# Performance work log

Hardware: AMD Instinct MI355X
Metric: run time of the kernel (lower is better)

The kernel has to match this reference:

```python
import jax, jax.numpy as jnp
import numpy as np

MAX_DELTAS = 4  # number of concurrently loaded delta adapters


def _dequant(qw, qz, sc):
    """GPTQ-style 4-bit dequant with a single group (g_idx == 0).

    qw: [D, O, K//8] int32, 8 x 4-bit values packed along the input (K) dim.
    qz: [D, O//8, 1] int32, 8 x 4-bit zero points packed along the output dim.
    sc: [D, O, 1] float scales (one group).
    Returns dense delta weights [D, O, K].
    """
    shifts = jnp.arange(8, dtype=jnp.int32) * 4
    D, O, Kp = qw.shape
    w = ((qw[:, :, :, None] >> shifts) & 0xF).reshape(D, O, Kp * 8)   # [D,O,K]
    z = ((qz[:, :, 0][:, :, None] >> shifts) & 0xF).reshape(D, O)     # [D,O]
    return (w.astype(sc.dtype) - (z.astype(sc.dtype) + 1.0)[:, :, None]) * sc


def setup_inputs() -> dict:
    key = jax.random.key(0)
    ks = jax.random.split(key, 16)
    T, IN = 1024, 4096
    Q, KV = 4096, 1024  # 32 q-heads, 8 kv-heads, head_size 128
    OUT = Q + 2 * KV    # 6144
    D, PACK = MAX_DELTAS, 8
    IMAX = np.int32(2**31 - 1)
    return {
        "x": jax.random.normal(ks[0], (T, IN), dtype=jnp.float32),
        "w_base": jax.random.normal(ks[1], (OUT, IN), dtype=jnp.float32) * 0.02,
        "bias": jax.random.normal(ks[2], (OUT,), dtype=jnp.float32) * 0.02,
        "qweight_q": jax.random.randint(ks[3], (D, Q, IN // PACK), 0, IMAX, dtype=jnp.int32),
        "qweight_k": jax.random.randint(ks[4], (D, KV, IN // PACK), 0, IMAX, dtype=jnp.int32),
        "qweight_v": jax.random.randint(ks[5], (D, KV, IN // PACK), 0, IMAX, dtype=jnp.int32),
        "qzeros_q": jax.random.randint(ks[6], (D, Q // PACK, 1), 0, IMAX, dtype=jnp.int32),
        "qzeros_k": jax.random.randint(ks[7], (D, KV // PACK, 1), 0, IMAX, dtype=jnp.int32),
        "qzeros_v": jax.random.randint(ks[8], (D, KV // PACK, 1), 0, IMAX, dtype=jnp.int32),
        "scales_q": jax.random.uniform(ks[9], (D, Q, 1), dtype=jnp.float32) * 0.01,
        "scales_k": jax.random.uniform(ks[10], (D, KV, 1), dtype=jnp.float32) * 0.01,
        "scales_v": jax.random.uniform(ks[11], (D, KV, 1), dtype=jnp.float32) * 0.01,
        "indices": jax.random.randint(ks[12], (T,), 0, D, dtype=jnp.int32),
    }


def reference(x, w_base, bias, qweight_q, qweight_k, qweight_v,
              qzeros_q, qzeros_k, qzeros_v, scales_q, scales_k, scales_v,
              indices):
    # Base fused QKV projection.
    out = x @ w_base.T + bias  # [T, OUT]
    # Dequantize the three packed delta stacks and concatenate along out dim,
    # matching the (q, k, v) output_slices scatter of apply_delta.
    Wd = jnp.concatenate([
        _dequant(qweight_q, qzeros_q, scales_q),
        _dequant(qweight_k, qzeros_k, scales_k),
        _dequant(qweight_v, qzeros_v, scales_v),
    ], axis=1)  # [D, OUT, IN]
    # Per-token indexed delta matmul: token t uses adapter indices[t].
    for d in range(MAX_DELTAS):
        xm = jnp.where((indices == d)[:, None], x, 0.0)  # [T, IN]
        out = out + xm @ Wd[d].T
    return out
```

## Files before the change

kernel.cpp:

```cpp
#include <hip/hip_runtime.h>
#include <stdint.h>

#define T_TOK 1024
#define K_IN  4096
#define N_OUT 6144
#define N_Q   4096
#define N_KV  1024
#define N_D   4
#define KP    512

#define TM 64
#define TN 128
#define BK 64
#define NSTEPS (K_IN / BK)
#define PM_MAX 1280
#define MT (PM_MAX/TM)
#define NT (N_OUT/TN)
#define NBLK (NT * MT)

#define NB_WB ((N_OUT * K_IN / 8) / 256)
#define NB_RP (48 * 4 * 2 * 8)
#define NB_XP (PM_MAX * 2)

typedef __attribute__((ext_vector_type(8)))  short  short8;
typedef __attribute__((ext_vector_type(4)))  float  float4v;
typedef __attribute__((ext_vector_type(4)))  float  f32x4;
typedef __attribute__((ext_vector_type(4)))  uint   u32x4;

__device__ __forceinline__ ushort f2bf(float f) {
    uint32_t u = __float_as_uint(f);
    u = (u + 0x7FFFu + ((u >> 16) & 1u)) >> 16;
    return (ushort)u;
}
__device__ __forceinline__ uint pack2(ushort a, ushort b) {
    return (uint)a | ((uint)b << 16);
}

__device__ __forceinline__ short8 unpack_nib(uint q) {
    union { u32x4 u; short8 s; } r;
    uint t1 = q >> 8, t2 = q >> 16, t3 = q >> 24;
    r.u.x = ((q  & 0xFu) | ((q  & 0xF0u) << 12)) | 0x43004300u;
    r.u.y = ((t1 & 0xFu) | ((t1 & 0xF0u) << 12)) | 0x43004300u;
    r.u.z = ((t2 & 0xFu) | ((t2 & 0xF0u) << 12)) | 0x43004300u;
    r.u.w = ((t3 & 0xFu) | ((t3 & 0xF0u) << 12)) | 0x43004300u;
    return r.s;
}

__global__ void build_perm_kernel(const int* __restrict__ indices,
                                  int* __restrict__ perm,
                                  int* __restrict__ pofs) {
    __shared__ int cw[16][4];
    __shared__ int pw[16][4];
    __shared__ int ps[N_D + 1];
    int tid = threadIdx.x;
    for (int p = tid; p < PM_MAX; p += 1024) perm[p] = -1;

    int d = indices[tid];
    unsigned long long m[4];
    m[0] = __ballot(d == 0); m[1] = __ballot(d == 1);
    m[2] = __ballot(d == 2); m[3] = __ballot(d == 3);
    int lane = tid & 63, wv = tid >> 6;
    if (lane < 4) cw[wv][lane] = (int)__popcll(m[lane]);
    __syncthreads();
    if (tid == 0) {
        int tot[4] = {0, 0, 0, 0};
        for (int w = 0; w < 16; w++)
            for (int dd = 0; dd < 4; dd++) { pw[w][dd] = tot[dd]; tot[dd] += cw[w][dd]; }
        int run = 0;
        for (int dd = 0; dd < N_D; dd++) { ps[dd] = run; run += ((tot[dd] + TM - 1) / TM) * TM; }
        ps[N_D] = run;
        for (int dd = 0; dd <= N_D; dd++) pofs[dd] = ps[dd];
    }
    __syncthreads();
    unsigned long long lt = (1ull << lane) - 1ull;
    int rank = pw[wv][d] + (int)__popcll(m[d] & lt);
    perm[ps[d] + rank] = tid;
}

__global__ void prep_kernel(const float* __restrict__ w_base, ushort* __restrict__ wb16,
                            const int* __restrict__ qw_q, const int* __restrict__ qw_k,
                            const int* __restrict__ qw_v, uint* __restrict__ qp,
                            const float* __restrict__ x, const int* __restrict__ perm,
                            ushort* __restrict__ xp, float* __restrict__ rs) {
    __shared__ int slds[64 * 64];
    int tid = threadIdx.x;
    int b = blockIdx.x;

    if (b < NB_WB) {
        int id = b * 256 + tid;
        const f32x4* src = (const f32x4*)(w_base + (size_t)id * 8);
        f32x4 a = __builtin_nontemporal_load(src);
        f32x4 c = __builtin_nontemporal_load(src + 1);
        u32x4 packv;
        packv.x = pack2(f2bf(a.x), f2bf(a.y));
        packv.y = pack2(f2bf(a.z), f2bf(a.w));
        packv.z = pack2(f2bf(c.x), f2bf(c.y));
        packv.w = pack2(f2bf(c.z), f2bf(c.w));
        *(u32x4*)(wb16 + (size_t)id * 8) = packv;
        return;
    }
    b -= NB_WB;
    if (b < NB_RP) {
        int s8 = b & 7;
        int r  = b >> 3;
        int w2 = r & 1; r >>= 1;
        int d  = r & 3;
        int bn = r >> 2;
        const int* qw; int r0, Osec;
        if (bn < 32)      { qw = qw_q; r0 = bn * 128;        Osec = N_Q;  }
        else if (bn < 40) { qw = qw_k; r0 = (bn - 32) * 128; Osec = N_KV; }
        else              { qw = qw_v; r0 = (bn - 40) * 128; Osec = N_KV; }
#pragma unroll
        for (int k = 0; k < 4; k++) {
            int p   = k * 256 + tid;
            int row = p >> 4, c4 = p & 15;
            const int* src = qw + ((size_t)d * Osec + r0 + w2 * 64 + row) * KP + s8 * 64 + c4 * 4;
            *(u32x4*)&slds[row * 64 + c4 * 4] = *(const u32x4*)src;
        }
        __syncthreads();
        size_t obase = (size_t)b * 4096;
#pragma unroll
        for (int k = 0; k < 2; k++) {
            int p    = k * 256 + tid;
            int sl   = p >> 6, lane = p & 63;
            int quad = lane >> 4, l16 = lane & 15;
            uint pk[8];
#pragma unroll
            for (int e = 0; e < 8; e++) {
                int jj = e >> 1, h = e & 1;
                pk[e] = (uint)slds[(jj * 16 + l16) * 64 + sl * 8 + h * 4 + quad];
            }
            *(u32x4*)(qp + obase + (size_t)p * 8)     = *(u32x4*)&pk[0];
            *(u32x4*)(qp + obase + (size_t)p * 8 + 4) = *(u32x4*)&pk[4];
        }
        return;
    }
    b -= NB_RP;
    {
        int pm = b >> 1;
        int half = b & 1;
        int c0 = half * (K_IN / 2) + tid * 8;
        int tok = perm[pm];
        ushort res[8];
        if (tok < 0) {
#pragma unroll
            for (int j = 0; j < 8; j++) res[j] = 0;
        } else {
            const f32x4* src = (const f32x4*)(x + (size_t)tok * K_IN + c0);
            f32x4 a = __builtin_nontemporal_load(src);
            f32x4 c = __builtin_nontemporal_load(src + 1);
            float v[8] = {a.x, a.y, a.z, a.w, c.x, c.y, c.z, c.w};
#pragma unroll
            for (int j = 0; j < 8; j++) res[j] = f2bf(v[j]);
        }
        u32x4 packv;
        packv.x = pack2(res[0], res[1]); packv.y = pack2(res[2], res[3]);
        packv.z = pack2(res[4], res[5]); packv.w = pack2(res[6], res[7]);
        *(u32x4*)(xp + (size_t)pm * K_IN + c0) = packv;

        float ssum = 0.f;
#pragma unroll
        for (int j = 0; j < 8; j++) ssum += __uint_as_float((uint)res[j] << 16);
#pragma unroll
        for (int off = 32; off > 0; off >>= 1) ssum += __shfl_xor(ssum, off);
        float* wsum = (float*)slds;
        if ((tid & 63) == 0) wsum[tid >> 6] = ssum;
        __syncthreads();
        if (tid == 0) rs[pm * 2 + half] = wsum[0] + wsum[1] + wsum[2] + wsum[3];
    }
}

__global__ __launch_bounds__(256, 3) void gemm_kernel(
    const ushort* __restrict__ xp, const ushort* __restrict__ wb16,
    const uint* __restrict__ qp,
    const int* __restrict__ qz_q, const int* __restrict__ qz_k, const int* __restrict__ qz_v,
    const float* __restrict__ sc_q, const float* __restrict__ sc_k, const float* __restrict__ sc_v,
    const float* __restrict__ bias,
    const int* __restrict__ perm, const int* __restrict__ pofs,
    const float* __restrict__ rs,
    float* __restrict__ out) {

    __shared__ ushort As[2][TM * BK];
    __shared__ ushort Bs[2][TN * BK];

    int lin  = blockIdx.x;
    int low3 = lin & 7, rest = lin >> 3;
    int bm   = rest % MT, bq = rest / MT;
    int bn   = bq * 8 + low3;

    int m0 = bm * TM, n0 = bn * TN;
    int ptot = pofs[N_D];
    if (m0 >= ptot) return;
    int d = 0;
    while (d < N_D - 1 && m0 >= pofs[d + 1]) d++;

    int tid  = threadIdx.x;
    int lane = tid & 63;
    int wv   = tid >> 6;
    int wm   = (wv & 1) * 32;
    int wn   = (wv >> 1) * 64;
    int quad = lane >> 4;
    int l16  = lane & 15;
    int xa   = l16 & 7;

    const uint* qpw = qp + (((size_t)(bn * 4 + d) * 2 + (wv >> 1)) * 64 * 64 * 8)
                         + (size_t)lane * 8;

    const float4v zero4 = {0.f, 0.f, 0.f, 0.f};
    float4v acc_b[2][4], acc_d[2][4];
#pragma unroll
    for (int i = 0; i < 2; i++)
#pragma unroll
        for (int jj = 0; jj < 4; jj++) { acc_b[i][jj] = zero4; acc_d[i][jj] = zero4; }

    auto stage = [&](ushort* dstA, ushort* dstB, int k0) {
#pragma unroll
        for (int w = 0; w < 2; w++) {
            int p   = w * 256 + tid;
            int row = p >> 3;
            int ckl = (p & 7) ^ (row & 7);
            const ushort* ga = xp + (size_t)(m0 + row) * K_IN + k0 + ckl * 8;
            int base = (w * 256 + (tid & ~63)) * 8;
            __builtin_amdgcn_global_load_lds((const __attribute__((address_space(1))) void*)ga,
                                             (__attribute__((address_space(3))) void*)(dstA + base), 16, 0, 0);
        }
#pragma unroll
        for (int w = 0; w < 4; w++) {
            int p   = w * 256 + tid;
            int row = p >> 3;
            int ckl = (p & 7) ^ (row & 7);
            const ushort* gb = wb16 + (size_t)(n0 + row) * K_IN + k0 + ckl * 8;
            int base = (w * 256 + (tid & ~63)) * 8;
            __builtin_amdgcn_global_load_lds((const __attribute__((address_space(1))) void*)gb,
                                             (__attribute__((address_space(3))) void*)(dstB + base), 16, 0, 0);
        }
    };

    int buf = 0;
    stage(As[0], Bs[0], 0);
    uint q_cur[8];
    *(u32x4*)&q_cur[0] = *(const u32x4*)(qpw);
    *(u32x4*)&q_cur[4] = *(const u32x4*)(qpw + 4);
    __syncthreads();

    for (int s = 0; s < NSTEPS; s++) {
        uint q_nxt[8];
        if (s + 1 < NSTEPS) {
            stage(As[1 - buf], Bs[1 - buf], (s + 1) * BK);
            const uint* qn = qpw + (size_t)(s + 1) * 512;
            *(u32x4*)&q_nxt[0] = *(const u32x4*)(qn);
            *(u32x4*)&q_nxt[4] = *(const u32x4*)(qn + 4);
        }

        const ushort* Ab = As[buf];
        const ushort* Bb = Bs[buf];
#pragma unroll
        for (int kk = 0; kk < BK; kk += 32) {
            int h   = kk >> 5;
            int ckb = (kk >> 3) + quad;
            short8 a[2], b[4], bd[4];
#pragma unroll
            for (int i = 0; i < 2; i++)
                a[i] = *(const short8*)(Ab + (wm + i * 16 + l16) * BK + (ckb ^ xa) * 8);
#pragma unroll
            for (int jj = 0; jj < 4; jj++)
                b[jj] = *(const short8*)(Bb + (wn + jj * 16 + l16) * BK + (ckb ^ xa) * 8);
#pragma unroll
            for (int jj = 0; jj < 4; jj++)
                bd[jj] = unpack_nib(q_cur[jj * 2 + h]);
#pragma unroll
            for (int i = 0; i < 2; i++)
#pragma unroll
                for (int jj = 0; jj < 4; jj++) {
                    acc_b[i][jj] = __builtin_amdgcn_mfma_f32_16x16x32_bf16(a[i], b[jj],  acc_b[i][jj], 0, 0, 0);
                    acc_d[i][jj] = __builtin_amdgcn_mfma_f32_16x16x32_bf16(a[i], bd[jj], acc_d[i][jj], 0, 0, 0);
                }
        }
        __syncthreads();
#pragma unroll
        for (int e = 0; e < 8; e++) q_cur[e] = q_nxt[e];
        buf ^= 1;
    }

    const int* qz; const float* sc; int r0, Osec;
    if (n0 < N_Q)            { qz = qz_q; sc = sc_q; r0 = n0;                Osec = N_Q;  }
    else if (n0 < N_Q + N_KV){ qz = qz_k; sc = sc_k; r0 = n0 - N_Q;          Osec = N_KV; }
    else                     { qz = qz_v; sc = sc_v; r0 = n0 - (N_Q + N_KV); Osec = N_KV; }

    float s4[4], cc4[4], bv4[4];
#pragma unroll
    for (int jj = 0; jj < 4; jj++) {
        int rsec = r0 + wn + jj * 16 + l16;
        float sv = sc[(size_t)d * Osec + rsec];
        int   zq = qz[(size_t)d * (Osec >> 3) + (rsec >> 3)];
        int   z  = (zq >> ((rsec & 7) * 4)) & 0xF;
        s4[jj]  = sv;
        cc4[jj] = sv * (float)(129 + z);
        bv4[jj] = bias[n0 + wn + jj * 16 + l16];
    }
#pragma unroll
    for (int i = 0; i < 2; i++) {
        int toks[4]; float rsv[4];
#pragma unroll
        for (int r = 0; r < 4; r++) {
            int row = m0 + wm + i * 16 + quad * 4 + r;
            toks[r] = perm[row];
            rsv[r]  = rs[row * 2] + rs[row * 2 + 1];
        }
#pragma unroll
        for (int jj = 0; jj < 4; jj++) {
            int col = n0 + wn + jj * 16 + l16;
#pragma unroll
            for (int r = 0; r < 4; r++) {
                int tok = toks[r];
                if (tok >= 0) {
                    float v = bv4[jj] + acc_b[i][jj][r] + s4[jj] * acc_d[i][jj][r] - cc4[jj] * rsv[r];
                    out[(size_t)tok * N_OUT + col] = v;
                }
            }
        }
    }
}

extern "C" void kernel_launch(void* const* d_in, const int* in_sizes, int n_in,
                              void* d_out, int out_size, void* d_ws, size_t ws_size,
                              hipStream_t stream) {
    const float* x      = (const float*)d_in[0];
    const float* w_base = (const float*)d_in[1];
    const float* bias   = (const float*)d_in[2];
    const int*   qw_q   = (const int*)d_in[3];
    const int*   qw_k   = (const int*)d_in[4];
    const int*   qw_v   = (const int*)d_in[5];
    const int*   qz_q   = (const int*)d_in[6];
    const int*   qz_k   = (const int*)d_in[7];
    const int*   qz_v   = (const int*)d_in[8];
    const float* sc_q   = (const float*)d_in[9];
    const float* sc_k   = (const float*)d_in[10];
    const float* sc_v   = (const float*)d_in[11];
    const int*   indices= (const int*)d_in[12];
    float* out = (float*)d_out;

    char* ws = (char*)d_ws;
    ushort* wb16 = (ushort*)ws;
    size_t wb_bytes = (size_t)N_OUT * K_IN * 2;
    ushort* xp = (ushort*)(ws + wb_bytes);
    size_t xp_bytes = (size_t)PM_MAX * K_IN * 2;
    float* rsum = (float*)(ws + wb_bytes + xp_bytes);
    size_t rs_bytes = (size_t)PM_MAX * 2 * sizeof(float);
    int* perm = (int*)(ws + wb_bytes + xp_bytes + rs_bytes);
    int* pofs = perm + PM_MAX;
    uint* qp  = (uint*)(ws + wb_bytes + xp_bytes + rs_bytes + PM_MAX * 4 + 64);

    build_perm_kernel<<<1, 1024, 0, stream>>>(indices, perm, pofs);
    prep_kernel<<<NB_WB + NB_RP + NB_XP, 256, 0, stream>>>(
        w_base, wb16, qw_q, qw_k, qw_v, qp, x, perm, xp, rsum);
    gemm_kernel<<<NBLK, 256, 0, stream>>>(xp, wb16, qp,
        qz_q, qz_k, qz_v, sc_q, sc_k, sc_v, bias,
        perm, pofs, rsum, out);
}
```

Baseline: 413.4 us.

## Fuse base-weight bf16 conversion into GEMM by staging fp32 w_base directly

Removes the separate prep pass that converted w_base to bf16 in workspace; the GEMM now streams fp32 w_base tiles into LDS and converts to bf16 per fragment at read time. This saves a full write and reread of the bf16 weight copy, but doubles LDS footprint and global traffic for B per tile across all M-tiles, and occupancy hint drops from 3 to 2 blocks. Also rewrites nibble unpacking with byte-permute instructions to cut ALU work.

```diff
diff --git a/kernel.cpp b/kernel.cpp
--- a/kernel.cpp
+++ b/kernel.cpp
@@ -1,4 +1,5 @@
 #include <hip/hip_runtime.h>
+#include <hip/hip_bf16.h>
 #include <stdint.h>
 
 #define T_TOK 1024
@@ -18,7 +19,6 @@
 #define NT (N_OUT/TN)
 #define NBLK (NT * MT)
 
-#define NB_WB ((N_OUT * K_IN / 8) / 256)
 #define NB_RP (48 * 4 * 2 * 8)
 #define NB_XP (PM_MAX * 2)
 
@@ -35,14 +35,20 @@
 __device__ __forceinline__ uint pack2(ushort a, ushort b) {
     return (uint)a | ((uint)b << 16);
 }
+__device__ __forceinline__ uint cvt2(float lo, float hi) {
+    union { __hip_bfloat162 h2; uint u; } c;
+    c.h2 = __float22bfloat162_rn(make_float2(lo, hi));
+    return c.u;
+}
 
 __device__ __forceinline__ short8 unpack_nib(uint q) {
     union { u32x4 u; short8 s; } r;
-    uint t1 = q >> 8, t2 = q >> 16, t3 = q >> 24;
-    r.u.x = ((q  & 0xFu) | ((q  & 0xF0u) << 12)) | 0x43004300u;
-    r.u.y = ((t1 & 0xFu) | ((t1 & 0xF0u) << 12)) | 0x43004300u;
-    r.u.z = ((t2 & 0xFu) | ((t2 & 0xF0u) << 12)) | 0x43004300u;
-    r.u.w = ((t3 & 0xFu) | ((t3 & 0xF0u) << 12)) | 0x43004300u;
+    uint e = q & 0x0F0F0F0Fu;
+    uint o = (q >> 4) & 0x0F0F0F0Fu;
+    r.u.x = __builtin_amdgcn_perm(o, e, 0x0C040C00u) | 0x43004300u;
+    r.u.y = __builtin_amdgcn_perm(o, e, 0x0C050C01u) | 0x43004300u;
+    r.u.z = __builtin_amdgcn_perm(o, e, 0x0C060C02u) | 0x43004300u;
+    r.u.w = __builtin_amdgcn_perm(o, e, 0x0C070C03u) | 0x43004300u;
     return r.s;
 }
 
@@ -77,8 +83,7 @@
     perm[ps[d] + rank] = tid;
 }
 
-__global__ void prep_kernel(const float* __restrict__ w_base, ushort* __restrict__ wb16,
-                            const int* __restrict__ qw_q, const int* __restrict__ qw_k,
+__global__ void prep_kernel(const int* __restrict__ qw_q, const int* __restrict__ qw_k,
                             const int* __restrict__ qw_v, uint* __restrict__ qp,
                             const float* __restrict__ x, const int* __restrict__ perm,
                             ushort* __restrict__ xp, float* __restrict__ rs) {
@@ -86,20 +91,6 @@
     int tid = threadIdx.x;
     int b = blockIdx.x;
 
-    if (b < NB_WB) {
-        int id = b * 256 + tid;
-        const f32x4* src = (const f32x4*)(w_base + (size_t)id * 8);
-        f32x4 a = __builtin_nontemporal_load(src);
-        f32x4 c = __builtin_nontemporal_load(src + 1);
-        u32x4 packv;
-        packv.x = pack2(f2bf(a.x), f2bf(a.y));
-        packv.y = pack2(f2bf(a.z), f2bf(a.w));
-        packv.z = pack2(f2bf(c.x), f2bf(c.y));
-        packv.w = pack2(f2bf(c.z), f2bf(c.w));
-        *(u32x4*)(wb16 + (size_t)id * 8) = packv;
-        return;
-    }
-    b -= NB_WB;
     if (b < NB_RP) {
         int s8 = b & 7;
         int r  = b >> 3;
@@ -170,8 +161,8 @@
     }
 }
 
-__global__ __launch_bounds__(256, 3) void gemm_kernel(
-    const ushort* __restrict__ xp, const ushort* __restrict__ wb16,
+__global__ __launch_bounds__(256, 2) void gemm_kernel(
+    const ushort* __restrict__ xp, const float* __restrict__ w_base,
     const uint* __restrict__ qp,
     const int* __restrict__ qz_q, const int* __restrict__ qz_k, const int* __restrict__ qz_v,
     const float* __restrict__ sc_q, const float* __restrict__ sc_k, const float* __restrict__ sc_v,
@@ -181,7 +172,7 @@
     float* __restrict__ out) {
 
     __shared__ ushort As[2][TM * BK];
-    __shared__ ushort Bs[2][TN * BK];
+    __shared__ float  Bs[2][TN * BK];
 
     int lin  = blockIdx.x;
     int low3 = lin & 7, rest = lin >> 3;
@@ -202,6 +193,7 @@
     int quad = lane >> 4;
     int l16  = lane & 15;
     int xa   = l16 & 7;
+    int xb   = (l16 & 7) << 1;
 
     const uint* qpw = qp + (((size_t)(bn * 4 + d) * 2 + (wv >> 1)) * 64 * 64 * 8)
                          + (size_t)lane * 8;
@@ -213,7 +205,7 @@
 #pragma unroll
         for (int jj = 0; jj < 4; jj++) { acc_b[i][jj] = zero4; acc_d[i][jj] = zero4; }
 
-    auto stage = [&](ushort* dstA, ushort* dstB, int k0) {
+    auto stage = [&](ushort* dstA, float* dstB, int k0) {
 #pragma unroll
         for (int w = 0; w < 2; w++) {
             int p   = w * 256 + tid;
@@ -225,12 +217,12 @@
                                              (__attribute__((address_space(3))) void*)(dstA + base), 16, 0, 0);
         }
 #pragma unroll
-        for (int w = 0; w < 4; w++) {
+        for (int w = 0; w < 8; w++) {
             int p   = w * 256 + tid;
-            int row = p >> 3;
-            int ckl = (p & 7) ^ (row & 7);
-            const ushort* gb = wb16 + (size_t)(n0 + row) * K_IN + k0 + ckl * 8;
-            int base = (w * 256 + (tid & ~63)) * 8;
+            int row = p >> 4;
+            int ckl = (p & 15) ^ ((row & 7) << 1);
+            const float* gb = w_base + (size_t)(n0 + row) * K_IN + k0 + ckl * 4;
+            int base = (w * 256 + (tid & ~63)) * 4;
             __builtin_amdgcn_global_load_lds((const __attribute__((address_space(1))) void*)gb,
                                              (__attribute__((address_space(3))) void*)(dstB + base), 16, 0, 0);
         }
@@ -253,7 +245,7 @@
         }
 
         const ushort* Ab = As[buf];
-        const ushort* Bb = Bs[buf];
+        const float*  Bb = Bs[buf];
 #pragma unroll
         for (int kk = 0; kk < BK; kk += 32) {
             int h   = kk >> 5;
@@ -263,8 +255,16 @@
             for (int i = 0; i < 2; i++)
                 a[i] = *(const short8*)(Ab + (wm + i * 16 + l16) * BK + (ckb ^ xa) * 8);
 #pragma unroll
-            for (int jj = 0; jj < 4; jj++)
-                b[jj] = *(const short8*)(Bb + (wn + jj * 16 + l16) * BK + (ckb ^ xa) * 8);
+            for (int jj = 0; jj < 4; jj++) {
+                int pos = ((h << 3) + (quad << 1)) ^ xb;
+                const float* pB = Bb + (wn + jj * 16 + l16) * BK + pos * 4;
+                f32x4 f0 = *(const f32x4*)pB;
+                f32x4 f1 = *(const f32x4*)(pB + 4);
+                union { u32x4 u; short8 s8v; } bc;
+                bc.u.x = cvt2(f0.x, f0.y); bc.u.y = cvt2(f0.z, f0.w);
+                bc.u.z = cvt2(f1.x, f1.y); bc.u.w = cvt2(f1.z, f1.w);
+                b[jj] = bc.s8v;
+            }
 #pragma unroll
             for (int jj = 0; jj < 4; jj++)
                 bd[jj] = unpack_nib(q_cur[jj * 2 + h]);
@@ -341,20 +341,18 @@
     float* out = (float*)d_out;
 
     char* ws = (char*)d_ws;
-    ushort* wb16 = (ushort*)ws;
-    size_t wb_bytes = (size_t)N_OUT * K_IN * 2;
-    ushort* xp = (ushort*)(ws + wb_bytes);
+    ushort* xp = (ushort*)ws;
     size_t xp_bytes = (size_t)PM_MAX * K_IN * 2;
-    float* rsum = (float*)(ws + wb_bytes + xp_bytes);
+    float* rsum = (float*)(ws + xp_bytes);
     size_t rs_bytes = (size_t)PM_MAX * 2 * sizeof(float);
-    int* perm = (int*)(ws + wb_bytes + xp_bytes + rs_bytes);
+    int* perm = (int*)(ws + xp_bytes + rs_bytes);
     int* pofs = perm + PM_MAX;
-    uint* qp  = (uint*)(ws + wb_bytes + xp_bytes + rs_bytes + PM_MAX * 4 + 64);
+    uint* qp  = (uint*)(ws + xp_bytes + rs_bytes + PM_MAX * 4 + 64);
 
     build_perm_kernel<<<1, 1024, 0, stream>>>(indices, perm, pofs);
-    prep_kernel<<<NB_WB + NB_RP + NB_XP, 256, 0, stream>>>(
-        w_base, wb16, qw_q, qw_k, qw_v, qp, x, perm, xp, rsum);
-    gemm_kernel<<<NBLK, 256, 0, stream>>>(xp, wb16, qp,
+    prep_kernel<<<NB_RP + NB_XP, 256, 0, stream>>>(
+        qw_q, qw_k, qw_v, qp, x, perm, xp, rsum);
+    gemm_kernel<<<NBLK, 256, 0, stream>>>(xp, w_base, qp,
         qz_q, qz_k, qz_v, sc_q, sc_k, sc_v, bias,
         perm, pofs, rsum, out);
 }
```

Measured after the change: 465.8 us. +12.7%, slower.

## Triple-buffer LDS staging with explicit vmcnt waits and perm-based nibble unpack

Applied to the files above, without the earlier changes.

Replaces the double-buffered K loop with a three-stage LDS ring that keeps two tile loads in flight, unrolled by two with manual s_waitcnt vmcnt and raw s_barrier instead of __syncthreads. The packed delta weights are ping-ponged between two register sets. The 4-bit unpack now uses v_perm byte shuffles to cut ALU instructions. The third buffer adds LDS use, so launch bounds drop occupancy from 3 to 2 blocks per CU. The hand-counted vmcnt values risk race conditions if the count of outstanding loads is wrong.

```diff
diff --git a/kernel.cpp b/kernel.cpp
--- a/kernel.cpp
+++ b/kernel.cpp
@@ -38,11 +38,12 @@
 
 __device__ __forceinline__ short8 unpack_nib(uint q) {
     union { u32x4 u; short8 s; } r;
-    uint t1 = q >> 8, t2 = q >> 16, t3 = q >> 24;
-    r.u.x = ((q  & 0xFu) | ((q  & 0xF0u) << 12)) | 0x43004300u;
-    r.u.y = ((t1 & 0xFu) | ((t1 & 0xF0u) << 12)) | 0x43004300u;
-    r.u.z = ((t2 & 0xFu) | ((t2 & 0xF0u) << 12)) | 0x43004300u;
-    r.u.w = ((t3 & 0xFu) | ((t3 & 0xF0u) << 12)) | 0x43004300u;
+    uint e = q & 0x0F0F0F0Fu;
+    uint o = (q >> 4) & 0x0F0F0F0Fu;
+    r.u.x = __builtin_amdgcn_perm(o, e, 0x0C040C00u) | 0x43004300u;
+    r.u.y = __builtin_amdgcn_perm(o, e, 0x0C050C01u) | 0x43004300u;
+    r.u.z = __builtin_amdgcn_perm(o, e, 0x0C060C02u) | 0x43004300u;
+    r.u.w = __builtin_amdgcn_perm(o, e, 0x0C070C03u) | 0x43004300u;
     return r.s;
 }
 
@@ -170,7 +171,7 @@
     }
 }
 
-__global__ __launch_bounds__(256, 3) void gemm_kernel(
+__global__ __launch_bounds__(256, 2) void gemm_kernel(
     const ushort* __restrict__ xp, const ushort* __restrict__ wb16,
     const uint* __restrict__ qp,
     const int* __restrict__ qz_q, const int* __restrict__ qz_k, const int* __restrict__ qz_v,
@@ -180,8 +181,8 @@
     const float* __restrict__ rs,
     float* __restrict__ out) {
 
-    __shared__ ushort As[2][TM * BK];
-    __shared__ ushort Bs[2][TN * BK];
+    __shared__ ushort As[3][TM * BK];
+    __shared__ ushort Bs[3][TN * BK];
 
     int lin  = blockIdx.x;
     int low3 = lin & 7, rest = lin >> 3;
@@ -236,24 +237,13 @@
         }
     };
 
-    int buf = 0;
-    stage(As[0], Bs[0], 0);
-    uint q_cur[8];
-    *(u32x4*)&q_cur[0] = *(const u32x4*)(qpw);
-    *(u32x4*)&q_cur[4] = *(const u32x4*)(qpw + 4);
-    __syncthreads();
-
-    for (int s = 0; s < NSTEPS; s++) {
-        uint q_nxt[8];
-        if (s + 1 < NSTEPS) {
-            stage(As[1 - buf], Bs[1 - buf], (s + 1) * BK);
-            const uint* qn = qpw + (size_t)(s + 1) * 512;
-            *(u32x4*)&q_nxt[0] = *(const u32x4*)(qn);
-            *(u32x4*)&q_nxt[4] = *(const u32x4*)(qn + 4);
-        }
-
-        const ushort* Ab = As[buf];
-        const ushort* Bb = Bs[buf];
+    auto qload = [&](uint* qdst, int step) {
+        const uint* qn = qpw + (size_t)step * 512;
+        *(u32x4*)&qdst[0] = *(const u32x4*)(qn);
+        *(u32x4*)&qdst[4] = *(const u32x4*)(qn + 4);
+    };
+
+    auto compute = [&](const ushort* Ab, const ushort* Bb, const uint* qc) {
 #pragma unroll
         for (int kk = 0; kk < BK; kk += 32) {
             int h   = kk >> 5;
@@ -261,13 +251,13 @@
             short8 a[2], b[4], bd[4];
 #pragma unroll
             for (int i = 0; i < 2; i++)
-                a[i] = *(const short8*)(Ab + (wm + i * 16 + l16) * BK + (ckb ^ xa) * 8);
+                a[i] = *(const short8*)(Ab + (wm + i * 16 + l16) * BK + ((ckb ^ xa) * 8));
 #pragma unroll
             for (int jj = 0; jj < 4; jj++)
-                b[jj] = *(const short8*)(Bb + (wn + jj * 16 + l16) * BK + (ckb ^ xa) * 8);
+                b[jj] = *(const short8*)(Bb + (wn + jj * 16 + l16) * BK + ((ckb ^ xa) * 8));
 #pragma unroll
             for (int jj = 0; jj < 4; jj++)
-                bd[jj] = unpack_nib(q_cur[jj * 2 + h]);
+                bd[jj] = unpack_nib(qc[jj * 2 + h]);
 #pragma unroll
             for (int i = 0; i < 2; i++)
 #pragma unroll
@@ -276,10 +266,38 @@
                     acc_d[i][jj] = __builtin_amdgcn_mfma_f32_16x16x32_bf16(a[i], bd[jj], acc_d[i][jj], 0, 0, 0);
                 }
         }
-        __syncthreads();
-#pragma unroll
-        for (int e = 0; e < 8; e++) q_cur[e] = q_nxt[e];
-        buf ^= 1;
+    };
+
+    uint qA[8], qB[8];
+
+    qload(qA, 0);
+    stage(As[0], Bs[0], 0);
+    stage(As[1], Bs[1], BK);
+    asm volatile("s_waitcnt vmcnt(6)" ::: "memory");
+    __builtin_amdgcn_s_barrier();
+
+    int b0 = 0, b1 = 1, b2 = 2;
+#pragma unroll 1
+    for (int s = 0; s < NSTEPS; s += 2) {
+        qload(qB, s + 1);
+        __builtin_amdgcn_sched_barrier(0);
+        if (s + 2 < NSTEPS) stage(As[b2], Bs[b2], (s + 2) * BK);
+        compute(As[b0], Bs[b0], qA);
+        if (s < NSTEPS - 2)       asm volatile("s_waitcnt vmcnt(8)" ::: "memory");
+        else                      asm volatile("s_waitcnt vmcnt(2)" ::: "memory");
+        __builtin_amdgcn_s_barrier();
+
+        if (s + 2 < NSTEPS) {
+            qload(qA, s + 2);
+            __builtin_amdgcn_sched_barrier(0);
+        }
+        if (s + 3 < NSTEPS) stage(As[b0], Bs[b0], (s + 3) * BK);
+        compute(As[b1], Bs[b1], qB);
+        if (s + 1 < NSTEPS - 2)      asm volatile("s_waitcnt vmcnt(8)" ::: "memory");
+        else if (s + 1 == NSTEPS - 2) asm volatile("s_waitcnt vmcnt(2)" ::: "memory");
+        if (s + 1 < NSTEPS - 1) __builtin_amdgcn_s_barrier();
+
+        int t = b0; b0 = b2; b2 = b1; b1 = t;
     }
 
     const int* qz; const float* sc; int r0, Osec;
```

New measurement: 363.7 us. 1.14x faster.
